# Performance work log

Hardware: AMD Instinct MI355X
Metric: run time of the kernel (lower is better)

Reference implementation:

```python
import jax, jax.numpy as jnp
import numpy as np

TEMPERATURE = 0.07
HIDDEN = 512
PROJ = 128
B = 65536
K = 8  # negative_samples
EPS_LN = 1e-5


def _project(x, W1, b1, W2, b2, g, beta):
    # Linear(512,256) -> ReLU -> Linear(256,128) -> LayerNorm(128) -> L2 normalize
    h = jax.nn.relu(x @ W1 + b1)
    p = h @ W2 + b2
    mu = jnp.mean(p, axis=-1, keepdims=True)
    var = jnp.var(p, axis=-1, keepdims=True)
    p = (p - mu) * jax.lax.rsqrt(var + EPS_LN) * g + beta
    return p / jnp.linalg.norm(p, axis=-1, keepdims=True)


def setup_inputs() -> dict:
    key = jax.random.key(0)
    ks = jax.random.split(key, 8)
    hidden_states = jax.random.normal(ks[0], (B, HIDDEN), dtype=jnp.float32)
    positive_hidden = jax.random.normal(ks[1], (B, HIDDEN), dtype=jnp.float32)
    neg_idx = jax.random.randint(ks[2], (B, K), 0, 2 * B)
    W1 = jax.random.normal(ks[3], (HIDDEN, HIDDEN // 2), dtype=jnp.float32) / np.sqrt(HIDDEN)
    b1 = jnp.zeros((HIDDEN // 2,), dtype=jnp.float32)
    W2 = jax.random.normal(ks[4], (HIDDEN // 2, PROJ), dtype=jnp.float32) / np.sqrt(HIDDEN // 2)
    b2 = jnp.zeros((PROJ,), dtype=jnp.float32)
    ln_gamma = jnp.ones((PROJ,), dtype=jnp.float32)
    ln_beta = jnp.zeros((PROJ,), dtype=jnp.float32)
    return {
        "hidden_states": hidden_states,
        "positive_hidden": positive_hidden,
        "neg_idx": neg_idx,
        "W1": W1, "b1": b1, "W2": W2, "b2": b2,
        "ln_gamma": ln_gamma, "ln_beta": ln_beta,
    }


def reference(hidden_states, positive_hidden, neg_idx, W1, b1, W2, b2, ln_gamma, ln_beta):
    anchors = _project(hidden_states, W1, b1, W2, b2, ln_gamma, ln_beta)      # [B, PROJ]
    positives = _project(positive_hidden, W1, b1, W2, b2, ln_gamma, ln_beta)  # [B, PROJ]
    pool = jnp.concatenate([anchors, positives], axis=0)                       # [2B, PROJ]
    negs = pool[neg_idx]                                                      # [B, K, PROJ]
    pos_sim = jnp.sum(anchors * positives, axis=-1) / TEMPERATURE             # [B]
    neg_sims = jnp.einsum("bd,bkd->bk", anchors, negs) / TEMPERATURE         # [B, K]
    all_sims = jnp.concatenate([pos_sim[:, None], neg_sims], axis=1)          # [B, 1+K]
    loss = -pos_sim + jax.scipy.special.logsumexp(all_sims, axis=1)           # [B]
    return jnp.mean(loss)
```

## Files before the change

kernel.cpp:

```cpp
#include <hip/hip_runtime.h>

#define NB   65536
#define HID  512
#define MID  256
#define PROJ 128
#define KNEG 8
#define TEMP_INV (1.0f/0.07f)

typedef __attribute__((ext_vector_type(8))) short bf16x8;
typedef __attribute__((ext_vector_type(4))) float f32x4;

#define A_STR 520
#define H_STR 264
#define P_STR 132

__device__ __forceinline__ short f2bf(float x) {
    unsigned u = __float_as_uint(x);
    unsigned r = (u + 0x7fffu + ((u >> 16) & 1u)) >> 16;
    return (short)r;
}
__device__ __forceinline__ float bf2f(short h) {
    return __uint_as_float(((unsigned)(unsigned short)h) << 16);
}

__global__ void prep_w_kernel(const float* __restrict__ W, short* __restrict__ hi,
                              short* __restrict__ lo, int N, int Kshift, int total)
{
    int idx = blockIdx.x * 256 + threadIdx.x;
    if (idx >= total) return;
    int n = idx >> Kshift;
    int k = idx & ((1 << Kshift) - 1);
    float x = W[(size_t)k * N + n];
    short h = f2bf(x);
    short l = f2bf(x - bf2f(h));
    hi[idx] = h;
    lo[idx] = l;
}

__global__ __launch_bounds__(256, 2)
void proj_mfma(const float* __restrict__ hs, const float* __restrict__ ph,
               const short* __restrict__ w1h, const short* __restrict__ w1l,
               const short* __restrict__ w2h, const short* __restrict__ w2l,
               const float* __restrict__ b1, const float* __restrict__ b2,
               const float* __restrict__ gam, const float* __restrict__ bet,
               float* __restrict__ pool)
{
    __shared__ float smem[16640];
    short* Ahi = (short*)smem;
    short* Alo = Ahi + 32 * A_STR;
    short* Hhi = (short*)smem;
    short* Hlo = Hhi + 32 * H_STR;
    float* P   = smem + (32 * H_STR);

    const int tid  = threadIdx.x;
    const int w    = tid >> 6;
    const int lane = tid & 63;
    const int l16  = lane & 15;
    const int g    = lane >> 4;
    const int row0 = blockIdx.x * 32;
    const float* __restrict__ X = (row0 < NB) ? (hs + (size_t)row0 * HID)
                                              : (ph + (size_t)(row0 - NB) * HID);

    #pragma unroll
    for (int i = 0; i < 16; ++i) {
        const int f = i * 1024 + tid * 4;
        const int r = f >> 9, c = f & 511;
        float4 v = *reinterpret_cast<const float4*>(X + f);
        float xv[4] = {v.x, v.y, v.z, v.w};
        short hh[4], ll[4];
        #pragma unroll
        for (int j = 0; j < 4; ++j) {
            hh[j] = f2bf(xv[j]);
            ll[j] = f2bf(xv[j] - bf2f(hh[j]));
        }
        *reinterpret_cast<short4*>(Ahi + r * A_STR + c) = make_short4(hh[0], hh[1], hh[2], hh[3]);
        *reinterpret_cast<short4*>(Alo + r * A_STR + c) = make_short4(ll[0], ll[1], ll[2], ll[3]);
    }

    float b1v[4];
    #pragma unroll
    for (int nb = 0; nb < 4; ++nb) b1v[nb] = b1[w * 64 + nb * 16 + l16];

    __syncthreads();

    f32x4 acc[2][4];
    #pragma unroll
    for (int mb = 0; mb < 2; ++mb)
        #pragma unroll
        for (int nb = 0; nb < 4; ++nb) acc[mb][nb] = (f32x4){0.f, 0.f, 0.f, 0.f};

    const int koff = g * 8;
    for (int t = 0; t < 16; ++t) {
        const int k0 = t * 32 + koff;
        bf16x8 a_h[2], a_l[2], b_h[4], b_l[4];
        #pragma unroll
        for (int mb = 0; mb < 2; ++mb) {
            const int ro = (mb * 16 + l16) * A_STR + k0;
            a_h[mb] = *reinterpret_cast<const bf16x8*>(Ahi + ro);
            a_l[mb] = *reinterpret_cast<const bf16x8*>(Alo + ro);
        }
        #pragma unroll
        for (int nb = 0; nb < 4; ++nb) {
            const size_t co = (size_t)(w * 64 + nb * 16 + l16) * 512 + k0;
            b_h[nb] = *reinterpret_cast<const bf16x8*>(w1h + co);
            b_l[nb] = *reinterpret_cast<const bf16x8*>(w1l + co);
        }
        #pragma unroll
        for (int mb = 0; mb < 2; ++mb)
            #pragma unroll
            for (int nb = 0; nb < 4; ++nb) {
                acc[mb][nb] = __builtin_amdgcn_mfma_f32_16x16x32_bf16(a_h[mb], b_h[nb], acc[mb][nb], 0, 0, 0);
                acc[mb][nb] = __builtin_amdgcn_mfma_f32_16x16x32_bf16(a_h[mb], b_l[nb], acc[mb][nb], 0, 0, 0);
                acc[mb][nb] = __builtin_amdgcn_mfma_f32_16x16x32_bf16(a_l[mb], b_h[nb], acc[mb][nb], 0, 0, 0);
            }
    }

    __syncthreads();

    #pragma unroll
    for (int mb = 0; mb < 2; ++mb)
        #pragma unroll
        for (int nb = 0; nb < 4; ++nb) {
            const int col = w * 64 + nb * 16 + l16;
            #pragma unroll
            for (int r = 0; r < 4; ++r) {
                const int row = mb * 16 + g * 4 + r;
                float hval = fmaxf(acc[mb][nb][r] + b1v[nb], 0.f);
                short hh = f2bf(hval);
                short hl = f2bf(hval - bf2f(hh));
                Hhi[row * H_STR + col] = hh;
                Hlo[row * H_STR + col] = hl;
            }
        }

    __syncthreads();

    f32x4 acc2[2][2];
    #pragma unroll
    for (int mb = 0; mb < 2; ++mb)
        #pragma unroll
        for (int nb = 0; nb < 2; ++nb) acc2[mb][nb] = (f32x4){0.f, 0.f, 0.f, 0.f};

    for (int t = 0; t < 8; ++t) {
        const int k0 = t * 32 + koff;
        bf16x8 a_h[2], a_l[2], b_h[2], b_l[2];
        #pragma unroll
        for (int mb = 0; mb < 2; ++mb) {
            const int ro = (mb * 16 + l16) * H_STR + k0;
            a_h[mb] = *reinterpret_cast<const bf16x8*>(Hhi + ro);
            a_l[mb] = *reinterpret_cast<const bf16x8*>(Hlo + ro);
        }
        #pragma unroll
        for (int nb = 0; nb < 2; ++nb) {
            const size_t co = (size_t)(w * 32 + nb * 16 + l16) * 256 + k0;
            b_h[nb] = *reinterpret_cast<const bf16x8*>(w2h + co);
            b_l[nb] = *reinterpret_cast<const bf16x8*>(w2l + co);
        }
        #pragma unroll
        for (int mb = 0; mb < 2; ++mb)
            #pragma unroll
            for (int nb = 0; nb < 2; ++nb) {
                acc2[mb][nb] = __builtin_amdgcn_mfma_f32_16x16x32_bf16(a_h[mb], b_h[nb], acc2[mb][nb], 0, 0, 0);
                acc2[mb][nb] = __builtin_amdgcn_mfma_f32_16x16x32_bf16(a_h[mb], b_l[nb], acc2[mb][nb], 0, 0, 0);
                acc2[mb][nb] = __builtin_amdgcn_mfma_f32_16x16x32_bf16(a_l[mb], b_h[nb], acc2[mb][nb], 0, 0, 0);
            }
    }

    #pragma unroll
    for (int mb = 0; mb < 2; ++mb)
        #pragma unroll
        for (int nb = 0; nb < 2; ++nb) {
            const int col = w * 32 + nb * 16 + l16;
            #pragma unroll
            for (int r = 0; r < 4; ++r) {
                const int row = mb * 16 + g * 4 + r;
                P[row * P_STR + col] = acc2[mb][nb][r];
            }
        }

    __syncthreads();

    {
        const int tm = tid >> 5;
        const int tn = tid & 31;
        float4 g4  = *reinterpret_cast<const float4*>(gam + tn * 4);
        float4 be4 = *reinterpret_cast<const float4*>(bet + tn * 4);
        float4 b24 = *reinterpret_cast<const float4*>(b2  + tn * 4);
        float gf[4]  = {g4.x, g4.y, g4.z, g4.w};
        float bf[4]  = {be4.x, be4.y, be4.z, be4.w};
        float b2f[4] = {b24.x, b24.y, b24.z, b24.w};

        #pragma unroll
        for (int i = 0; i < 4; ++i) {
            float4 pv = *reinterpret_cast<const float4*>(P + (tm * 4 + i) * P_STR + tn * 4);
            float v[4] = {pv.x, pv.y, pv.z, pv.w};
            float lsum = 0.f, lsq = 0.f;
            #pragma unroll
            for (int j = 0; j < 4; ++j) {
                v[j] += b2f[j];
                lsum += v[j];
                lsq  += v[j] * v[j];
            }
            #pragma unroll
            for (int m = 1; m < 32; m <<= 1) {
                lsum += __shfl_xor(lsum, m, 64);
                lsq  += __shfl_xor(lsq,  m, 64);
            }
            float mu   = lsum * (1.0f / PROJ);
            float var  = lsq  * (1.0f / PROJ) - mu * mu;
            float rstd = rsqrtf(var + 1e-5f);
            float l2 = 0.f;
            #pragma unroll
            for (int j = 0; j < 4; ++j) {
                v[j] = (v[j] - mu) * rstd * gf[j] + bf[j];
                l2 += v[j] * v[j];
            }
            #pragma unroll
            for (int m = 1; m < 32; m <<= 1) l2 += __shfl_xor(l2, m, 64);
            float rn = rsqrtf(l2);
            float4 o;
            o.x = v[0] * rn; o.y = v[1] * rn; o.z = v[2] * rn; o.w = v[3] * rn;
            *reinterpret_cast<float4*>(pool + (size_t)(row0 + tm * 4 + i) * PROJ + tn * 4) = o;
        }
    }
}

__global__ __launch_bounds__(256, 4)
void loss_kernel(const float* __restrict__ pool, const int* __restrict__ nidx,
                 float* __restrict__ partials)
{
    const int wave = threadIdx.x >> 6;
    const int lane = threadIdx.x & 63;
    float local = 0.f;

    for (int b = blockIdx.x * 4 + wave; b < NB; b += gridDim.x * 4) {
        const float2 av = *reinterpret_cast<const float2*>(pool + (size_t)b * PROJ + lane * 2);
        const float2 pv = *reinterpret_cast<const float2*>(pool + (size_t)(b + NB) * PROJ + lane * 2);
        float d[9];
        d[0] = av.x * pv.x + av.y * pv.y;
        #pragma unroll
        for (int k = 0; k < KNEG; k++) {
            const int idx = nidx[b * KNEG + k];
            const float2 nv = *reinterpret_cast<const float2*>(pool + (size_t)idx * PROJ + lane * 2);
            d[k + 1] = av.x * nv.x + av.y * nv.y;
        }
        #pragma unroll
        for (int m = 1; m < 64; m <<= 1)
            #pragma unroll
            for (int t = 0; t < 9; t++) d[t] += __shfl_xor(d[t], m, 64);

        float pos = d[0] * TEMP_INV;
        float mx = pos;
        #pragma unroll
        for (int t = 1; t < 9; t++) mx = fmaxf(mx, d[t] * TEMP_INV);
        float se = 0.f;
        #pragma unroll
        for (int t = 0; t < 9; t++) se += __expf(d[t] * TEMP_INV - mx);
        float loss = -pos + mx + __logf(se);
        if (lane == 0) local += loss;
    }

    __shared__ float red[4];
    if (lane == 0) red[wave] = local;
    __syncthreads();
    if (threadIdx.x == 0)
        partials[blockIdx.x] = red[0] + red[1] + red[2] + red[3];
}

__global__ __launch_bounds__(256)
void reduce_kernel(const float* __restrict__ partials, float* __restrict__ out)
{
    const int tid = threadIdx.x;
    float s = 0.f;
    for (int i = tid; i < 4096; i += 256) s += partials[i];
    #pragma unroll
    for (int m = 1; m < 64; m <<= 1) s += __shfl_xor(s, m, 64);
    __shared__ float red[4];
    if ((tid & 63) == 0) red[tid >> 6] = s;
    __syncthreads();
    if (tid == 0)
        out[0] = (red[0] + red[1] + red[2] + red[3]) * (1.0f / NB);
}

extern "C" void kernel_launch(void* const* d_in, const int* in_sizes, int n_in,
                              void* d_out, int out_size, void* d_ws, size_t ws_size,
                              hipStream_t stream)
{
    const float* hs = (const float*)d_in[0];
    const float* ph = (const float*)d_in[1];
    const int*   ni = (const int*)  d_in[2];
    const float* W1 = (const float*)d_in[3];
    const float* b1 = (const float*)d_in[4];
    const float* W2 = (const float*)d_in[5];
    const float* b2 = (const float*)d_in[6];
    const float* gm = (const float*)d_in[7];
    const float* bt = (const float*)d_in[8];

    float* pool     = (float*)d_ws;
    float* partials = pool + (size_t)2 * NB * PROJ;
    short* w1h = (short*)(partials + 4096);
    short* w1l = w1h + HID * MID;
    short* w2h = w1l + HID * MID;
    short* w2l = w2h + MID * PROJ;
    float* out = (float*)d_out;

    prep_w_kernel<<<(HID * MID + 255) / 256, 256, 0, stream>>>(W1, w1h, w1l, MID, 9, HID * MID);
    prep_w_kernel<<<(MID * PROJ + 255) / 256, 256, 0, stream>>>(W2, w2h, w2l, PROJ, 8, MID * PROJ);

    proj_mfma<<<2 * NB / 32, 256, 0, stream>>>(hs, ph, w1h, w1l, w2h, w2l, b1, b2, gm, bt, pool);
    loss_kernel<<<4096, 256, 0, stream>>>(pool, ni, partials);
    reduce_kernel<<<1, 256, 0, stream>>>(partials, out);
}
```

Measured before the change: 636.0 us.

## Chunk projection K-dimension to shrink LDS and double occupancy; half-wave loss rows

The first GEMM now stages the 32x512 input tile in four 128-column chunks instead of all at once, cutting shared memory from about 66KB to about 33KB. This lets the launch bound request 4 blocks per CU instead of 2, to hide global-load latency. The cost is extra barriers per chunk, plus the P buffer now aliases the H buffer, which needs a barrier before P is written. The loss kernel now gives each half-wave one row with float4 loads, halving the shuffle-reduction steps per row.

```diff
diff --git a/kernel.cpp b/kernel.cpp
--- a/kernel.cpp
+++ b/kernel.cpp
@@ -10,7 +10,7 @@
 typedef __attribute__((ext_vector_type(8))) short bf16x8;
 typedef __attribute__((ext_vector_type(4))) float f32x4;
 
-#define A_STR 520
+#define A_STR 136
 #define H_STR 264
 #define P_STR 132
 
@@ -37,7 +37,7 @@
     lo[idx] = l;
 }
 
-__global__ __launch_bounds__(256, 2)
+__global__ __launch_bounds__(256, 4)
 void proj_mfma(const float* __restrict__ hs, const float* __restrict__ ph,
                const short* __restrict__ w1h, const short* __restrict__ w1l,
                const short* __restrict__ w2h, const short* __restrict__ w2l,
@@ -45,12 +45,12 @@
                const float* __restrict__ gam, const float* __restrict__ bet,
                float* __restrict__ pool)
 {
-    __shared__ float smem[16640];
+    __shared__ float smem[8448];
     short* Ahi = (short*)smem;
     short* Alo = Ahi + 32 * A_STR;
     short* Hhi = (short*)smem;
     short* Hlo = Hhi + 32 * H_STR;
-    float* P   = smem + (32 * H_STR);
+    float* P   = smem;
 
     const int tid  = threadIdx.x;
     const int w    = tid >> 6;
@@ -61,28 +61,10 @@
     const float* __restrict__ X = (row0 < NB) ? (hs + (size_t)row0 * HID)
                                               : (ph + (size_t)(row0 - NB) * HID);
 
-    #pragma unroll
-    for (int i = 0; i < 16; ++i) {
-        const int f = i * 1024 + tid * 4;
-        const int r = f >> 9, c = f & 511;
-        float4 v = *reinterpret_cast<const float4*>(X + f);
-        float xv[4] = {v.x, v.y, v.z, v.w};
-        short hh[4], ll[4];
-        #pragma unroll
-        for (int j = 0; j < 4; ++j) {
-            hh[j] = f2bf(xv[j]);
-            ll[j] = f2bf(xv[j] - bf2f(hh[j]));
-        }
-        *reinterpret_cast<short4*>(Ahi + r * A_STR + c) = make_short4(hh[0], hh[1], hh[2], hh[3]);
-        *reinterpret_cast<short4*>(Alo + r * A_STR + c) = make_short4(ll[0], ll[1], ll[2], ll[3]);
-    }
-
     float b1v[4];
     #pragma unroll
     for (int nb = 0; nb < 4; ++nb) b1v[nb] = b1[w * 64 + nb * 16 + l16];
 
-    __syncthreads();
-
     f32x4 acc[2][4];
     #pragma unroll
     for (int mb = 0; mb < 2; ++mb)
@@ -90,29 +72,51 @@
         for (int nb = 0; nb < 4; ++nb) acc[mb][nb] = (f32x4){0.f, 0.f, 0.f, 0.f};
 
     const int koff = g * 8;
-    for (int t = 0; t < 16; ++t) {
-        const int k0 = t * 32 + koff;
-        bf16x8 a_h[2], a_l[2], b_h[4], b_l[4];
-        #pragma unroll
-        for (int mb = 0; mb < 2; ++mb) {
-            const int ro = (mb * 16 + l16) * A_STR + k0;
-            a_h[mb] = *reinterpret_cast<const bf16x8*>(Ahi + ro);
-            a_l[mb] = *reinterpret_cast<const bf16x8*>(Alo + ro);
-        }
-        #pragma unroll
-        for (int nb = 0; nb < 4; ++nb) {
-            const size_t co = (size_t)(w * 64 + nb * 16 + l16) * 512 + k0;
-            b_h[nb] = *reinterpret_cast<const bf16x8*>(w1h + co);
-            b_l[nb] = *reinterpret_cast<const bf16x8*>(w1l + co);
-        }
-        #pragma unroll
-        for (int mb = 0; mb < 2; ++mb)
+    for (int c = 0; c < 4; ++c) {
+        __syncthreads();
+        #pragma unroll
+        for (int i = 0; i < 4; ++i) {
+            const int f = i * 256 + tid;
+            const int r = f >> 5, c4 = (f & 31) * 4;
+            float4 v = *reinterpret_cast<const float4*>(X + (size_t)r * HID + c * 128 + c4);
+            float xv[4] = {v.x, v.y, v.z, v.w};
+            short hh[4], ll[4];
+            #pragma unroll
+            for (int j = 0; j < 4; ++j) {
+                hh[j] = f2bf(xv[j]);
+                ll[j] = f2bf(xv[j] - bf2f(hh[j]));
+            }
+            *reinterpret_cast<short4*>(Ahi + r * A_STR + c4) = make_short4(hh[0], hh[1], hh[2], hh[3]);
+            *reinterpret_cast<short4*>(Alo + r * A_STR + c4) = make_short4(ll[0], ll[1], ll[2], ll[3]);
+        }
+        __syncthreads();
+
+        #pragma unroll
+        for (int t = 0; t < 4; ++t) {
+            const int kl = t * 32 + koff;
+            const int kg = c * 128 + kl;
+            bf16x8 a_h[2], a_l[2], b_h[4], b_l[4];
+            #pragma unroll
+            for (int mb = 0; mb < 2; ++mb) {
+                const int ro = (mb * 16 + l16) * A_STR + kl;
+                a_h[mb] = *reinterpret_cast<const bf16x8*>(Ahi + ro);
+                a_l[mb] = *reinterpret_cast<const bf16x8*>(Alo + ro);
+            }
             #pragma unroll
             for (int nb = 0; nb < 4; ++nb) {
-                acc[mb][nb] = __builtin_amdgcn_mfma_f32_16x16x32_bf16(a_h[mb], b_h[nb], acc[mb][nb], 0, 0, 0);
-                acc[mb][nb] = __builtin_amdgcn_mfma_f32_16x16x32_bf16(a_h[mb], b_l[nb], acc[mb][nb], 0, 0, 0);
-                acc[mb][nb] = __builtin_amdgcn_mfma_f32_16x16x32_bf16(a_l[mb], b_h[nb], acc[mb][nb], 0, 0, 0);
-            }
+                const size_t co = (size_t)(w * 64 + nb * 16 + l16) * 512 + kg;
+                b_h[nb] = *reinterpret_cast<const bf16x8*>(w1h + co);
+                b_l[nb] = *reinterpret_cast<const bf16x8*>(w1l + co);
+            }
+            #pragma unroll
+            for (int mb = 0; mb < 2; ++mb)
+                #pragma unroll
+                for (int nb = 0; nb < 4; ++nb) {
+                    acc[mb][nb] = __builtin_amdgcn_mfma_f32_16x16x32_bf16(a_h[mb], b_h[nb], acc[mb][nb], 0, 0, 0);
+                    acc[mb][nb] = __builtin_amdgcn_mfma_f32_16x16x32_bf16(a_h[mb], b_l[nb], acc[mb][nb], 0, 0, 0);
+                    acc[mb][nb] = __builtin_amdgcn_mfma_f32_16x16x32_bf16(a_l[mb], b_h[nb], acc[mb][nb], 0, 0, 0);
+                }
+        }
     }
 
     __syncthreads();
@@ -141,6 +145,7 @@
         #pragma unroll
         for (int nb = 0; nb < 2; ++nb) acc2[mb][nb] = (f32x4){0.f, 0.f, 0.f, 0.f};
 
+    #pragma unroll
     for (int t = 0; t < 8; ++t) {
         const int k0 = t * 32 + koff;
         bf16x8 a_h[2], a_l[2], b_h[2], b_l[2];
@@ -165,6 +170,8 @@
                 acc2[mb][nb] = __builtin_amdgcn_mfma_f32_16x16x32_bf16(a_l[mb], b_h[nb], acc2[mb][nb], 0, 0, 0);
             }
     }
+
+    __syncthreads();
 
     #pragma unroll
     for (int mb = 0; mb < 2; ++mb)
@@ -231,23 +238,25 @@
 {
     const int wave = threadIdx.x >> 6;
     const int lane = threadIdx.x & 63;
+    const int sub  = lane >> 5;
+    const int l32  = lane & 31;
     float local = 0.f;
 
-    for (int b = blockIdx.x * 4 + wave; b < NB; b += gridDim.x * 4) {
-        const float2 av = *reinterpret_cast<const float2*>(pool + (size_t)b * PROJ + lane * 2);
-        const float2 pv = *reinterpret_cast<const float2*>(pool + (size_t)(b + NB) * PROJ + lane * 2);
+    for (int b = blockIdx.x * 8 + wave * 2 + sub; b < NB; b += gridDim.x * 8) {
+        const float4 av = *reinterpret_cast<const float4*>(pool + (size_t)b * PROJ + l32 * 4);
+        const float4 pv = *reinterpret_cast<const float4*>(pool + (size_t)(b + NB) * PROJ + l32 * 4);
         float d[9];
-        d[0] = av.x * pv.x + av.y * pv.y;
+        d[0] = av.x * pv.x + av.y * pv.y + av.z * pv.z + av.w * pv.w;
         #pragma unroll
         for (int k = 0; k < KNEG; k++) {
             const int idx = nidx[b * KNEG + k];
-            const float2 nv = *reinterpret_cast<const float2*>(pool + (size_t)idx * PROJ + lane * 2);
-            d[k + 1] = av.x * nv.x + av.y * nv.y;
-        }
-        #pragma unroll
-        for (int m = 1; m < 64; m <<= 1)
-            #pragma unroll
-            for (int t = 0; t < 9; t++) d[t] += __shfl_xor(d[t], m, 64);
+            const float4 nv = *reinterpret_cast<const float4*>(pool + (size_t)idx * PROJ + l32 * 4);
+            d[k + 1] = av.x * nv.x + av.y * nv.y + av.z * nv.z + av.w * nv.w;
+        }
+        #pragma unroll
+        for (int m = 1; m < 32; m <<= 1)
+            #pragma unroll
+            for (int t = 0; t < 9; t++) d[t] += __shfl_xor(d[t], m, 32);
 
         float pos = d[0] * TEMP_INV;
         float mx = pos;
@@ -257,8 +266,10 @@
         #pragma unroll
         for (int t = 0; t < 9; t++) se += __expf(d[t] * TEMP_INV - mx);
         float loss = -pos + mx + __logf(se);
-        if (lane == 0) local += loss;
+        if (l32 == 0) local += loss;
     }
+
+    local += __shfl_xor(local, 32, 64);
 
     __shared__ float red[4];
     if (lane == 0) red[wave] = local;
```

After: 639.8 us. About the same (+0.6%).
